# Optimization experiments

Measured on AMD Instinct MI355X. Metric: run time of the kernel, lower is better.

The kernel has to match this reference:

```python
import jax, jax.numpy as jnp
import numpy as np
import math

B, QLEN, KLEN = 8, 128, 1024
KDIM = QDIM = ADIM = ODIM = 512
HM, HC = 4, 4            # monotonic / chunkwise heads
CHUNK = 4                # chunkwise attention window
EPS = 1e-6
SHARPENING = 1.0
NEG_INF = float(np.finfo(np.float32).min)


def moving_sum(x, back, forward):
    """Windowed sum over last axis: out[k] = sum_{j=k-back}^{k+forward} x[j].
    Equivalent to the conv1d-with-ones-filter moving_sum in the torch code."""
    K = x.shape[-1]
    xp = jnp.pad(x, [(0, 0)] * (x.ndim - 1) + [(back, forward)])
    cs = jnp.cumsum(xp, axis=-1)
    L = back + forward + 1
    upper = jax.lax.slice_in_dim(cs, L - 1, L - 1 + K, axis=-1)
    lower = jnp.concatenate([jnp.zeros_like(cs[..., :1]),
                             jax.lax.slice_in_dim(cs, 0, K - 1, axis=-1)], axis=-1)
    return upper - lower


def safe_cumprod(x, eps):
    """exp(exclusive_cumsum(log(clip(x, eps, 1)))) along last axis."""
    logx = jnp.log(jnp.clip(x, eps, 1.0))
    excl = jnp.concatenate([jnp.zeros_like(logx[..., :1]),
                            jnp.cumsum(logx, axis=-1)[..., :-1]], axis=-1)
    return jnp.exp(excl)


def _heads(x, w, b, h):
    y = x @ w + b                                   # [B, L, ADIM]
    bs, L, _ = y.shape
    return y.reshape(bs, L, h, -1).transpose(0, 2, 1, 3)  # [B, h, L, d_k]


def setup_inputs() -> dict:
    key = jax.random.key(0)
    ks = jax.random.split(key, 16)
    s = 0.02
    f32 = jnp.float32
    return {
        "key_x": jax.random.normal(ks[0], (B, KLEN, KDIM), f32),
        "query_x": jax.random.normal(ks[1], (B, QLEN, QDIM), f32),
        "mask": jnp.ones((B, QLEN, KLEN), jnp.int32),
        "wk_m": jax.random.normal(ks[2], (KDIM, ADIM), f32) * s,
        "bk_m": jnp.zeros((ADIM,), f32),
        "wq_m": jax.random.normal(ks[3], (QDIM, ADIM), f32) * s,
        "bq_m": jnp.zeros((ADIM,), f32),
        "r": jnp.asarray(-4.0, f32),
        "wk_c": jax.random.normal(ks[4], (KDIM, ADIM), f32) * s,
        "bk_c": jnp.zeros((ADIM,), f32),
        "wq_c": jax.random.normal(ks[5], (QDIM, ADIM), f32) * s,
        "bq_c": jnp.zeros((ADIM,), f32),
        "wv": jax.random.normal(ks[6], (KDIM, ADIM), f32) * s,
        "bv": jnp.zeros((ADIM,), f32),
        "wo": jax.random.normal(ks[7], (ADIM, ODIM), f32) * s,
        "bo": jnp.zeros((ODIM,), f32),
    }


def reference(key_x, query_x, mask, wk_m, bk_m, wq_m, bq_m, r,
              wk_c, bk_c, wq_c, bq_c, wv, bv, wo, bo):
    scale = math.sqrt(ADIM)
    m = (mask[:, None] > 0)                                    # [B,1,Q,K]

    # ---- monotonic energy (scaled_dot + offset r) ----
    km = _heads(key_x, wk_m, bk_m, HM)                         # [B,HM,K,dk]
    qm = _heads(query_x, wq_m, bq_m, HM)                       # [B,HM,Q,dk]
    e_mono = jnp.einsum('bhqd,bhkd->bhqk', qm, km) / scale + r
    e_mono = jnp.where(m, e_mono, NEG_INF)

    # ---- monotonic alpha via safe_cumprod + per-step cumsum recurrence ----
    p_choose = jax.nn.sigmoid(e_mono)                          # [B,HM,Q,K]
    cp = safe_cumprod(1.0 - p_choose, EPS)                     # [B,HM,Q,K]
    aw0 = jnp.zeros((B, HM, KLEN), e_mono.dtype).at[..., 0].set(1.0)

    def step(aw_prev, pc):
        p_i, cp_i = pc                                         # [B,HM,K]
        aw = p_i * cp_i * jnp.cumsum(aw_prev / jnp.maximum(cp_i, EPS), axis=-1)
        return aw, aw

    _, alpha = jax.lax.scan(step, aw0,
                            (p_choose.transpose(2, 0, 1, 3),
                             cp.transpose(2, 0, 1, 3)))
    alpha = alpha.transpose(1, 2, 0, 3)                        # [B,HM,Q,K]

    # ---- chunkwise energy ----
    kc = _heads(key_x, wk_c, bk_c, HC)
    qc = _heads(query_x, wq_c, bq_c, HC)
    e_chunk = jnp.einsum('bhqd,bhkd->bhqk', qc, kc) / scale
    e_chunk = jnp.where(m, e_chunk, NEG_INF)

    # ---- efficient chunkwise attention (clipped-logit trick) ----
    e = e_chunk - jnp.max(e_chunk, axis=-1, keepdims=True)
    sexp = jnp.maximum(jnp.exp(e), 1e-5)[:, None]              # [B,1,HC,Q,K]
    denom = moving_sum(sexp, CHUNK - 1, 0)                     # [B,1,HC,Q,K]
    beta = sexp * moving_sum(alpha[:, :, None] * SHARPENING / denom,
                             0, CHUNK - 1)                     # [B,HM,HC,Q,K]
    beta = beta.reshape(B, HM * HC, QLEN, KLEN)

    # ---- context + output projection ----
    v = (key_x @ wv + bv).reshape(B, KLEN, HM * HC, ADIM // (HM * HC))
    cv = jnp.einsum('bhqk,bkhd->bqhd', beta, v).reshape(B, QLEN, ADIM)
    return cv @ wo + bo
```

## Files before the change

### kernel.cpp

```cpp
#include <hip/hip_runtime.h>
#include <hip/hip_bf16.h>


#define NEG_INF (-3.402823466e38f)
#define EPS_MOCHA 1e-6f
#define INV_SCALE 0.04419417382415922f

typedef _Float16 half8 __attribute__((ext_vector_type(8)));
typedef _Float16 half4v __attribute__((ext_vector_type(4)));
typedef float f32x4 __attribute__((ext_vector_type(4)));

#define WAITBAR(N) asm volatile("s_waitcnt vmcnt(" #N ") lgkmcnt(0)\n\ts_barrier" ::: "memory")
#define BARLG() asm volatile("s_waitcnt lgkmcnt(0)\n\ts_barrier" ::: "memory")

__device__ __forceinline__ float frcp(float x) { return __builtin_amdgcn_rcpf(x); }

__device__ __forceinline__ float wave_incl_scan(float x)
{
    int v;
    v = __builtin_amdgcn_update_dpp(0, __builtin_bit_cast(int, x), 0x111, 0xF, 0xF, false);
    x += __builtin_bit_cast(float, v);
    v = __builtin_amdgcn_update_dpp(0, __builtin_bit_cast(int, x), 0x112, 0xF, 0xF, false);
    x += __builtin_bit_cast(float, v);
    v = __builtin_amdgcn_update_dpp(0, __builtin_bit_cast(int, x), 0x114, 0xF, 0xF, false);
    x += __builtin_bit_cast(float, v);
    v = __builtin_amdgcn_update_dpp(0, __builtin_bit_cast(int, x), 0x118, 0xF, 0xF, false);
    x += __builtin_bit_cast(float, v);
    v = __builtin_amdgcn_update_dpp(0, __builtin_bit_cast(int, x), 0x142, 0xA, 0xF, false);
    x += __builtin_bit_cast(float, v);
    v = __builtin_amdgcn_update_dpp(0, __builtin_bit_cast(int, x), 0x143, 0xC, 0xF, false);
    x += __builtin_bit_cast(float, v);
    return x;
}

__device__ __forceinline__ half8 cvt8(float4 a, float4 b)
{
    half8 h = {(_Float16)a.x, (_Float16)a.y, (_Float16)a.z, (_Float16)a.w,
               (_Float16)b.x, (_Float16)b.y, (_Float16)b.z, (_Float16)b.w};
    return h;
}

__global__ __launch_bounds__(256) void prep_all(
    const float* __restrict__ wk_m, const float* __restrict__ wk_c,
    const float* __restrict__ wv, const float* __restrict__ wq_m,
    const float* __restrict__ wq_c, const float* __restrict__ wo,
    const float* __restrict__ key_x, const float* __restrict__ query_x,
    _Float16* __restrict__ Wt5, _Float16* __restrict__ Wt_wo,
    _Float16* __restrict__ X16)
{
    __shared__ float T[64][65];
    const int bid = blockIdx.x;
    const int t = threadIdx.x;
    if (bid < 384) {
        const int z = bid >> 6, w = bid & 63;
        const float* W = (z == 0) ? wk_m : (z == 1) ? wk_c : (z == 2) ? wv
                       : (z == 3) ? wq_m : (z == 4) ? wq_c : wo;
        _Float16* O = (z < 5) ? (Wt5 + (size_t)z * 262144) : Wt_wo;
        const int n0 = (w & 7) * 64, k0 = (w >> 3) * 64;
        const int rr = t >> 4, cc = (t & 15) * 4;
#pragma unroll
        for (int r = 0; r < 4; ++r) {
            int k = r * 16 + rr;
            float4 v = *(const float4*)(W + (size_t)(k0 + k) * 512 + n0 + cc);
            T[k][cc + 0] = v.x; T[k][cc + 1] = v.y;
            T[k][cc + 2] = v.z; T[k][cc + 3] = v.w;
        }
        __syncthreads();
        const int nn = t >> 2, kc = (t & 3) * 16;
        _Float16 tmp[16];
#pragma unroll
        for (int i = 0; i < 16; ++i) tmp[i] = (_Float16)T[kc + i][nn];
        _Float16* Op = O + (size_t)(n0 + nn) * 512 + k0 + kc;
        *(half8*)(Op)     = *(half8*)&tmp[0];
        *(half8*)(Op + 8) = *(half8*)&tmp[8];
    } else {
        const size_t KELEMS = (size_t)8192 * 512;
        size_t o = ((size_t)(bid - 384) * 256 + t) * 8;
        const float* s = (o < KELEMS) ? (key_x + o) : (query_x + (o - KELEMS));
        float4 a = *(const float4*)s;
        float4 b = *(const float4*)(s + 4);
        *(half8*)(X16 + o) = cvt8(a, b);
    }
}

__device__ __forceinline__ void stage16(const _Float16* src, _Float16* dst)
{
    __builtin_amdgcn_global_load_lds(
        (const __attribute__((address_space(1))) void*)src,
        (__attribute__((address_space(3))) void*)dst, 16, 0, 0);
}

template <int NSTEPS>
__device__ __forceinline__ void gemm8_f16(
    const _Float16* __restrict__ Abase, const _Float16* __restrict__ Bbase,
    _Float16* As, _Float16* Bs, f32x4 acc[4][2])
{
    const int tid = threadIdx.x;
    const int lane = tid & 63, wave = tid >> 6;
    const int wm = wave >> 2, wn = wave & 3;
    const int col = lane & 15, quad = lane >> 4;
    const int r0 = tid >> 2, seg = tid & 3;

    const _Float16* Ag = Abase + (size_t)r0 * 512 + seg * 8;
    const _Float16* Bg = Bbase + (size_t)r0 * 512 + seg * 8;

    stage16(Ag, As + tid * 8);
    stage16(Bg, Bs + tid * 8);
    if (NSTEPS > 1) {
        stage16(Ag + 32, As + 4096 + tid * 8);
        stage16(Bg + 32, Bs + 4096 + tid * 8);
        WAITBAR(2);
    } else {
        WAITBAR(0);
    }

#pragma unroll
    for (int ks = 0; ks < NSTEPS; ++ks) {
        const int cur = ks % 3;
        if (ks + 2 < NSTEPS) {
            const int s2 = (ks + 2) % 3;
            stage16(Ag + (ks + 2) * 32, As + s2 * 4096 + tid * 8);
            stage16(Bg + (ks + 2) * 32, Bs + s2 * 4096 + tid * 8);
        }
        const _Float16* Afr = As + cur * 4096 + (size_t)(wm * 64 + col) * 32 + quad * 8;
        const _Float16* Bfr = Bs + cur * 4096 + (size_t)(wn * 32 + col) * 32 + quad * 8;
        half8 a[4], b[2];
#pragma unroll
        for (int t = 0; t < 4; ++t) a[t] = *(const half8*)(Afr + (size_t)t * 16 * 32);
#pragma unroll
        for (int t = 0; t < 2; ++t) b[t] = *(const half8*)(Bfr + (size_t)t * 16 * 32);
#pragma unroll
        for (int mt = 0; mt < 4; ++mt)
#pragma unroll
            for (int nt = 0; nt < 2; ++nt)
                acc[mt][nt] = __builtin_amdgcn_mfma_f32_16x16x32_f16(
                    a[mt], b[nt], acc[mt][nt], 0, 0, 0);
        if (ks + 2 < NSTEPS)      WAITBAR(2);
        else if (ks + 1 < NSTEPS) WAITBAR(0);
    }
}

__device__ __forceinline__ void proj_epilogue8(
    f32x4 acc[4][2], const float* __restrict__ bias, void* __restrict__ Cv,
    int m0, int n0, int f16o)
{
    const int tid = threadIdx.x;
    const int lane = tid & 63, wave = tid >> 6;
    const int wm = wave >> 2, wn = wave & 3;
    const int col = lane & 15, quad = lane >> 4;
    float bnt[2];
#pragma unroll
    for (int nt = 0; nt < 2; ++nt)
        bnt[nt] = bias[n0 + wn * 32 + nt * 16 + col];
#pragma unroll
    for (int mt = 0; mt < 4; ++mt) {
        const int rowb = m0 + wm * 64 + mt * 16 + quad * 4;
#pragma unroll
        for (int nt = 0; nt < 2; ++nt) {
            const int cc = n0 + wn * 32 + nt * 16 + col;
#pragma unroll
            for (int r = 0; r < 4; ++r) {
                float v = acc[mt][nt][r] + bnt[nt];
                if (f16o)
                    ((_Float16*)Cv)[(size_t)(rowb + r) * 512 + cc] = (_Float16)v;
                else
                    ((float*)Cv)[(size_t)(rowb + r) * 512 + cc] = v;
            }
        }
    }
}

__global__ __launch_bounds__(512, 8) void mfma_proj5(
    const _Float16* __restrict__ X16, const _Float16* __restrict__ Wt5,
    const float* __restrict__ b0, void* __restrict__ C0,
    const float* __restrict__ b1, void* __restrict__ C1,
    const float* __restrict__ b2, void* __restrict__ C2,
    const float* __restrict__ b3, void* __restrict__ C3,
    const float* __restrict__ b4, void* __restrict__ C4)
{
    __shared__ _Float16 As[12288];
    __shared__ _Float16 Bs[12288];
    const int bid = (blockIdx.x & 7) * 104 + (blockIdx.x >> 3);
    int g, mblk, nblk;
    if (bid < 768) {
        g = bid >> 8; mblk = (bid & 255) >> 2; nblk = bid & 3;
    } else {
        const int t = bid - 768;
        g = 3 + (t >> 5); mblk = (t & 31) >> 2; nblk = t & 3;
    }
    const bool qry = g >= 3;
    const _Float16* A = X16 + (qry ? (size_t)8192 * 512 : 0);
    const _Float16* Wt = Wt5 + (size_t)g * 262144;
    const float* bias = (g == 0) ? b0 : (g == 1) ? b1 : (g == 2) ? b2
                      : (g == 3) ? b3 : b4;
    void* Cv = (g == 0) ? C0 : (g == 1) ? C1 : (g == 2) ? C2
             : (g == 3) ? C3 : C4;
    const int m0 = mblk * 128, n0 = nblk * 128;

    f32x4 acc[4][2];
#pragma unroll
    for (int mt = 0; mt < 4; ++mt)
#pragma unroll
        for (int nt = 0; nt < 2; ++nt) acc[mt][nt] = (f32x4)0.f;
    gemm8_f16<16>(A + (size_t)m0 * 512, Wt + (size_t)n0 * 512, As, Bs, acc);
    proj_epilogue8(acc, bias, Cv, m0, n0, 1);
}

__global__ __launch_bounds__(512, 4) void mfma_proj_out(
    const _Float16* __restrict__ A16, const _Float16* __restrict__ Wt,
    const float* __restrict__ bias, float* __restrict__ C)
{
    __shared__ _Float16 As[12288];
    __shared__ _Float16 Bs[12288];
    const int m0 = blockIdx.x * 128, n0 = blockIdx.y * 128;
    f32x4 acc[4][2];
#pragma unroll
    for (int mt = 0; mt < 4; ++mt)
#pragma unroll
        for (int nt = 0; nt < 2; ++nt) acc[mt][nt] = (f32x4)0.f;
    gemm8_f16<16>(A16 + (size_t)m0 * 512, Wt + (size_t)n0 * 512, As, Bs, acc);
    proj_epilogue8(acc, bias, C, m0, n0, 0);
}

__global__ __launch_bounds__(512, 4) void energy_mfma(
    const _Float16* __restrict__ Qm, const _Float16* __restrict__ Km,
    const _Float16* __restrict__ Qc, const _Float16* __restrict__ Kc,
    const int* __restrict__ mask, float* __restrict__ e_mono,
    _Float16* __restrict__ e_chunk16, const float* __restrict__ r_ptr)
{
    __shared__ _Float16 As[12288];
    __shared__ _Float16 Bs[12288];
    const int tid = threadIdx.x;
    const int lane = tid & 63, wave = tid >> 6;
    const int wm = wave >> 2, wn = wave & 3;
    const int col = lane & 15, quad = lane >> 4;
    const int kt0 = blockIdx.x * 128;
    const int h = blockIdx.y;
    const int b = blockIdx.z;
    const float rv = r_ptr[0];
    const int r0 = tid >> 2, seg = tid & 3;

    const _Float16* Am0 = Qm + (size_t)(b * 128) * 512 + h * 128 + (size_t)r0 * 512 + seg * 8;
    const _Float16* Ac0 = Qc + (size_t)(b * 128) * 512 + h * 128 + (size_t)r0 * 512 + seg * 8;
    const _Float16* Bm0 = Km + (size_t)(b * 1024 + kt0) * 512 + h * 128 + (size_t)r0 * 512 + seg * 8;
    const _Float16* Bc0 = Kc + (size_t)(b * 1024 + kt0) * 512 + h * 128 + (size_t)r0 * 512 + seg * 8;
#define EGA(s) (((s) < 4 ? Am0 : Ac0) + ((s) & 3) * 32)
#define EGB(s) (((s) < 4 ? Bm0 : Bc0) + ((s) & 3) * 32)

    f32x4 accM[4][2], accC[4][2];
#pragma unroll
    for (int mt = 0; mt < 4; ++mt)
#pragma unroll
        for (int nt = 0; nt < 2; ++nt) { accM[mt][nt] = (f32x4)0.f; accC[mt][nt] = (f32x4)0.f; }

#pragma unroll
    for (int s = 0; s < 2; ++s) {
        stage16(EGA(s), As + s * 4096 + tid * 8);
        stage16(EGB(s), Bs + s * 4096 + tid * 8);
    }
    WAITBAR(2);

#pragma unroll
    for (int ks = 0; ks < 8; ++ks) {
        const int cur = ks % 3;
        if (ks + 2 < 8) {
            const int s2 = (ks + 2) % 3;
            stage16(EGA(ks + 2), As + s2 * 4096 + tid * 8);
            stage16(EGB(ks + 2), Bs + s2 * 4096 + tid * 8);
        }
        const _Float16* Afr = As + cur * 4096 + (size_t)(wm * 64 + col) * 32 + quad * 8;
        const _Float16* Bfr = Bs + cur * 4096 + (size_t)(wn * 32 + col) * 32 + quad * 8;
        half8 a[4], bf[2];
#pragma unroll
        for (int t = 0; t < 4; ++t) a[t]  = *(const half8*)(Afr + (size_t)t * 16 * 32);
#pragma unroll
        for (int t = 0; t < 2; ++t) bf[t] = *(const half8*)(Bfr + (size_t)t * 16 * 32);
        if (ks < 4) {
#pragma unroll
            for (int mt = 0; mt < 4; ++mt)
#pragma unroll
                for (int nt = 0; nt < 2; ++nt)
                    accM[mt][nt] = __builtin_amdgcn_mfma_f32_16x16x32_f16(a[mt], bf[nt], accM[mt][nt], 0, 0, 0);
        } else {
#pragma unroll
            for (int mt = 0; mt < 4; ++mt)
#pragma unroll
                for (int nt = 0; nt < 2; ++nt)
                    accC[mt][nt] = __builtin_amdgcn_mfma_f32_16x16x32_f16(a[mt], bf[nt], accC[mt][nt], 0, 0, 0);
        }
        if (ks + 2 < 8)      WAITBAR(2);
        else if (ks + 1 < 8) WAITBAR(0);
    }
#undef EGA
#undef EGB

#pragma unroll
    for (int mt = 0; mt < 4; ++mt) {
        const int qb = wm * 64 + mt * 16 + quad * 4;
#pragma unroll
        for (int nt = 0; nt < 2; ++nt) {
            const int kc = kt0 + wn * 32 + nt * 16 + col;
#pragma unroll
            for (int r = 0; r < 4; ++r) {
                const int q = qb + r;
                const int mv = mask[((size_t)b * 128 + q) * 1024 + kc];
                const size_t oi = (((size_t)b * 4 + h) * 128 + q) * 1024 + kc;
                float vm = accM[mt][nt][r] * INV_SCALE + rv;
                e_mono[oi] = mv ? vm : NEG_INF;
                float vc = accC[mt][nt][r] * INV_SCALE;
                e_chunk16[oi] = (_Float16)(mv ? vc : NEG_INF);
            }
        }
    }
}

__device__ __forceinline__ void transcend_row(
    const float* __restrict__ Erow, int lane, float o_pcp[16], float o_inv[16])
{
    const float* E = Erow + lane * 16;
    float e[16];
    *(float4*)&e[0]  = *(const float4*)(E);
    *(float4*)&e[4]  = *(const float4*)(E + 4);
    *(float4*)&e[8]  = *(const float4*)(E + 8);
    *(float4*)&e[12] = *(const float4*)(E + 12);

    float p[16], l[16];
#pragma unroll
    for (int i = 0; i < 16; ++i) {
        p[i] = frcp(1.f + __expf(-e[i]));
        l[i] = __logf(fmaxf(1.f - p[i], EPS_MOCHA));
    }
    float incl[16];
    incl[0] = l[0];
#pragma unroll
    for (int i = 1; i < 16; ++i) incl[i] = incl[i - 1] + l[i];
    float total = incl[15];
    float x = wave_incl_scan(total);
    float base = x - total;
#pragma unroll
    for (int i = 0; i < 16; ++i) {
        float cl = base + (i ? incl[i - 1] : 0.f);
        float cp = __expf(cl);
        o_pcp[i] = p[i] * cp;
        o_inv[i] = frcp(fmaxf(cp, EPS_MOCHA));
    }
}

#define SW2(k) ((k) + ((k) >> 4))

__global__ __launch_bounds__(512) void alpha_pre(
    const float* __restrict__ e_mono, float* __restrict__ G,
    float* __restrict__ pcp)
{
    __shared__ float pshare[8][1088];
    const int tid = threadIdx.x;
    const int lane = tid & 63;
    const int wid = tid >> 6;
    const int row = blockIdx.x * 8 + wid;
    const int q = row & 127;

    float pq[16], iq[16];
    transcend_row(e_mono + (size_t)row * 1024, lane, pq, iq);

    float* P = pcp + (size_t)row * 1024 + lane * 16;
    *(float4*)(P)      = *(float4*)&pq[0];
    *(float4*)(P + 4)  = *(float4*)&pq[4];
    *(float4*)(P + 8)  = *(float4*)&pq[8];
    *(float4*)(P + 12) = *(float4*)&pq[12];

#pragma unroll
    for (int i = 0; i < 16; ++i)
        pshare[wid][SW2(lane * 16 + i)] = pq[i];
    __syncthreads();

    float g[16];
    if (q == 0) {
#pragma unroll
        for (int i = 0; i < 16; ++i) g[i] = 0.f;
        if (lane == 0) g[0] = iq[0];
    } else if (wid > 0) {
#pragma unroll
        for (int i = 0; i < 16; ++i)
            g[i] = pshare[wid - 1][SW2(lane * 16 + i)] * iq[i];
    } else {
        float pm[16], im[16];
        transcend_row(e_mono + (size_t)(row - 1) * 1024, lane, pm, im);
#pragma unroll
        for (int i = 0; i < 16; ++i) g[i] = pm[i] * iq[i];
    }
    float* Gp = G + (size_t)row * 1024 + lane * 16;
    *(float4*)(Gp)      = *(float4*)&g[0];
    *(float4*)(Gp + 4)  = *(float4*)&g[4];
    *(float4*)(Gp + 8)  = *(float4*)&g[8];
    *(float4*)(Gp + 12) = *(float4*)&g[12];
}

__global__ __launch_bounds__(256) void alpha_scan(
    const float* __restrict__ G, float* __restrict__ S)
{
    __shared__ float carry[2][4];
    const int tid = threadIdx.x;
    const int lane = tid & 63, wid = tid >> 6;
    const int bh = blockIdx.x;
    const float* Gp = G + (size_t)bh * 131072 + tid * 4;
    float* Sp = S + (size_t)bh * 131072 + tid * 4;

    float4 g0 = *(const float4*)(Gp);
    float4 g1 = *(const float4*)(Gp + 1024);
    float4 g2 = *(const float4*)(Gp + 2048);
    float4 g3 = *(const float4*)(Gp + 3072);

    float Sv0 = 1.f, Sv1 = 1.f, Sv2 = 1.f, Sv3 = 1.f;

#define SCAN_STEP(GV, QQ)                                                    \
    {                                                                        \
        float i0 = GV.x * Sv0;                                               \
        float i1 = fmaf(GV.y, Sv1, i0);                                      \
        float i2 = fmaf(GV.z, Sv2, i1);                                      \
        float i3 = fmaf(GV.w, Sv3, i2);                                      \
        float x = wave_incl_scan(i3);                                        \
        float base = x - i3;                                                 \
        if (lane == 63) carry[(QQ) & 1][wid] = x;                            \
        BARLG();                                                             \
        float pre = 0.f;                                                     \
        if (wid > 0) pre += carry[(QQ) & 1][0];                              \
        if (wid > 1) pre += carry[(QQ) & 1][1];                              \
        if (wid > 2) pre += carry[(QQ) & 1][2];                              \
        float ba = pre + base;                                               \
        Sv0 = ba + i0; Sv1 = ba + i1; Sv2 = ba + i2; Sv3 = ba + i3;          \
        float4 sv = {Sv0, Sv1, Sv2, Sv3};                                    \
        *(float4*)(Sp + (size_t)(QQ) * 1024) = sv;                           \
    }

    for (int q = 0; q < 128; q += 4) {
        SCAN_STEP(g0, q);
        if (q + 4 < 128) g0 = *(const float4*)(Gp + (size_t)(q + 4) * 1024);
        SCAN_STEP(g1, q + 1);
        if (q + 5 < 128) g1 = *(const float4*)(Gp + (size_t)(q + 5) * 1024);
        SCAN_STEP(g2, q + 2);
        if (q + 6 < 128) g2 = *(const float4*)(Gp + (size_t)(q + 6) * 1024);
        SCAN_STEP(g3, q + 3);
        if (q + 7 < 128) g3 = *(const float4*)(Gp + (size_t)(q + 7) * 1024);
    }
#undef SCAN_STEP
}

__global__ __launch_bounds__(256) void beta_kernel(
    const _Float16* __restrict__ e_chunk16, const float* __restrict__ pcp,
    const float* __restrict__ S, _Float16* __restrict__ beta)
{
    __shared__ float red[4];
    __shared__ float edge_sx[4][4];
    __shared__ float edge_t[4][4][4];
    const int q = blockIdx.x, b = blockIdx.y;
    const int tid = threadIdx.x;
    const int lane = tid & 63, wid = tid >> 6;
    const int k4 = tid * 4;

    float av[4][4];
#pragma unroll
    for (int hm = 0; hm < 4; ++hm) {
        const size_t off = (((size_t)b * 4 + hm) * 128 + q) * 1024 + k4;
        float4 pv = *(const float4*)(pcp + off);
        float4 sv = *(const float4*)(S + off);
        av[hm][0] = pv.x * sv.x;
        av[hm][1] = pv.y * sv.y;
        av[hm][2] = pv.z * sv.z;
        av[hm][3] = pv.w * sv.w;
    }

    for (int hc = 0; hc < 4; ++hc) {
        half4v ev = *(const half4v*)(e_chunk16 + (((size_t)b * 4 + hc) * 128 + q) * 1024 + k4);
        float e[4] = {(float)ev[0], (float)ev[1], (float)ev[2], (float)ev[3]};

        float mx = fmaxf(fmaxf(e[0], e[1]), fmaxf(e[2], e[3]));
#pragma unroll
        for (int off = 32; off >= 1; off >>= 1)
            mx = fmaxf(mx, __shfl_xor(mx, off, 64));
        if (lane == 0) red[wid] = mx;
        __syncthreads();
        mx = fmaxf(fmaxf(red[0], red[1]), fmaxf(red[2], red[3]));

        float sx[4];
#pragma unroll
        for (int i = 0; i < 4; ++i)
            sx[i] = fmaxf(__expf(e[i] - mx), 1e-5f);
        if (lane == 63) {
            edge_sx[wid][0] = sx[0]; edge_sx[wid][1] = sx[1];
            edge_sx[wid][2] = sx[2]; edge_sx[wid][3] = sx[3];
        }
        __syncthreads();

        float p1 = __shfl_up(sx[3], 1, 64);
        float p2 = __shfl_up(sx[2], 1, 64);
        float p3 = __shfl_up(sx[1], 1, 64);
        if (lane == 0) {
            if (wid > 0) {
                p1 = edge_sx[wid - 1][3];
                p2 = edge_sx[wid - 1][2];
                p3 = edge_sx[wid - 1][1];
            } else {
                p1 = 0.f; p2 = 0.f; p3 = 0.f;
            }
        }
        float den[4];
        den[0] = sx[0] + p1 + p2 + p3;
        den[1] = sx[1] + sx[0] + p1 + p2;
        den[2] = sx[2] + sx[1] + sx[0] + p1;
        den[3] = sx[3] + sx[2] + sx[1] + sx[0];
        float rd[4];
#pragma unroll
        for (int i = 0; i < 4; ++i) rd[i] = frcp(den[i]);

        float t[4][4];
#pragma unroll
        for (int hm = 0; hm < 4; ++hm)
#pragma unroll
            for (int i = 0; i < 4; ++i)
                t[hm][i] = av[hm][i] * rd[i];
        if (lane == 0) {
#pragma unroll
            for (int hm = 0; hm < 4; ++hm) {
                edge_t[wid][hm][0] = t[hm][0]; edge_t[wid][hm][1] = t[hm][1];
                edge_t[wid][hm][2] = t[hm][2]; edge_t[wid][hm][3] = t[hm][3];
            }
        }
        __syncthreads();

#pragma unroll
        for (int hm = 0; hm < 4; ++hm) {
            float n1 = __shfl_down(t[hm][0], 1, 64);
            float n2 = __shfl_down(t[hm][1], 1, 64);
            float n3 = __shfl_down(t[hm][2], 1, 64);
            if (lane == 63) {
                if (wid < 3) {
                    n1 = edge_t[wid + 1][hm][0];
                    n2 = edge_t[wid + 1][hm][1];
                    n3 = edge_t[wid + 1][hm][2];
                } else {
                    n1 = 0.f; n2 = 0.f; n3 = 0.f;
                }
            }
            float o0 = sx[0] * (t[hm][0] + t[hm][1] + t[hm][2] + t[hm][3]);
            float o1 = sx[1] * (t[hm][1] + t[hm][2] + t[hm][3] + n1);
            float o2 = sx[2] * (t[hm][2] + t[hm][3] + n1 + n2);
            float o3 = sx[3] * (t[hm][3] + n1 + n2 + n3);
            _Float16* Brow = beta + (((size_t)b * 16 + hm * 4 + hc) * 128 + q) * 1024;
            half4v hv = {(_Float16)o0, (_Float16)o1, (_Float16)o2, (_Float16)o3};
            *(half4v*)(Brow + k4) = hv;
        }
    }
}

__global__ __launch_bounds__(256) void context_kernel(
    const _Float16* __restrict__ beta, const _Float16* __restrict__ V16,
    _Float16* __restrict__ cv16)
{
    __shared__ float bS[128][64];
    __shared__ float vS[128][32];
    const int qh = blockIdx.x, h = blockIdx.y, b = blockIdx.z;
    const int tid = threadIdx.x;
    const int ty = tid >> 3, tx = tid & 7;
    const int q0 = qh * 64;

    const _Float16* Bbase = beta + (((size_t)b * 16 + h) * 128 + q0) * 1024;
    const _Float16* Vbase = V16 + (size_t)b * 1024 * 512 + h * 32;

    float acc[2][4];
#pragma unroll
    for (int i = 0; i < 2; ++i)
#pragma unroll
        for (int j = 0; j < 4; ++j) acc[i][j] = 0.f;

    for (int k0 = 0; k0 < 1024; k0 += 128) {
        {
            int r = tid >> 2, c = tid & 3;
#pragma unroll
            for (int s = 0; s < 4; ++s) {
                half8 v = *(const half8*)(Bbase + (size_t)r * 1024 + k0 + s * 32 + c * 8);
#pragma unroll
                for (int j = 0; j < 8; ++j) bS[s * 32 + c * 8 + j][r] = (float)v[j];
            }
        }
        {
            int kk = tid >> 3, c = tid & 7;
#pragma unroll
            for (int s = 0; s < 4; ++s) {
                half4v v = *(const half4v*)(Vbase + (size_t)(k0 + s * 32 + kk) * 512 + c * 4);
                float4 f = {(float)v[0], (float)v[1], (float)v[2], (float)v[3]};
                *(float4*)&vS[s * 32 + kk][c * 4] = f;
            }
        }
        __syncthreads();
#pragma unroll 8
        for (int kk = 0; kk < 128; ++kk) {
            float a0 = bS[kk][ty * 2], a1 = bS[kk][ty * 2 + 1];
            float bb[4];
            *(float4*)bb = *(const float4*)&vS[kk][tx * 4];
#pragma unroll
            for (int j = 0; j < 4; ++j) {
                acc[0][j] = fmaf(a0, bb[j], acc[0][j]);
                acc[1][j] = fmaf(a1, bb[j], acc[1][j]);
            }
        }
        __syncthreads();
    }
#pragma unroll
    for (int i = 0; i < 2; ++i) {
        _Float16* Cp = cv16 + ((size_t)b * 128 + q0 + ty * 2 + i) * 512 + h * 32 + tx * 4;
        half4v hv = {(_Float16)acc[i][0], (_Float16)acc[i][1],
                     (_Float16)acc[i][2], (_Float16)acc[i][3]};
        *(half4v*)Cp = hv;
    }
}

extern "C" void kernel_launch(void* const* d_in, const int* in_sizes, int n_in,
                              void* d_out, int out_size, void* d_ws, size_t ws_size,
                              hipStream_t stream)
{
    const float* key_x   = (const float*)d_in[0];
    const float* query_x = (const float*)d_in[1];
    const int*   mask    = (const int*)d_in[2];
    const float* wk_m = (const float*)d_in[3];
    const float* bk_m = (const float*)d_in[4];
    const float* wq_m = (const float*)d_in[5];
    const float* bq_m = (const float*)d_in[6];
    const float* r    = (const float*)d_in[7];
    const float* wk_c = (const float*)d_in[8];
    const float* bk_c = (const float*)d_in[9];
    const float* wq_c = (const float*)d_in[10];
    const float* bq_c = (const float*)d_in[11];
    const float* wv   = (const float*)d_in[12];
    const float* bv   = (const float*)d_in[13];
    const float* wo   = (const float*)d_in[14];
    const float* bo   = (const float*)d_in[15];
    float* out = (float*)d_out;

    float* ws = (float*)d_ws;
    _Float16* hws = (_Float16*)d_ws;
    const size_t MEGF = 1024 * 1024;
    _Float16* Km16  = hws;
    _Float16* Kc16  = hws + 4 * MEGF;
    _Float16* Qm16  = hws + 8 * MEGF;
    _Float16* Qc16  = hws + 8 * MEGF + 524288;
    _Float16* X16   = hws + 16 * MEGF;
    float* e_mono  = ws + 11 * MEGF;
    _Float16* e_chunk16 = hws + 34 * MEGF;
    _Float16* V16  = hws + 38 * MEGF;
    float* G       = ws;
    float* pcp     = ws + 4 * MEGF;
    float* S       = ws + 23 * MEGF;
    _Float16* beta16 = hws + 16 * MEGF;
    _Float16* Wt5   = hws + 54 * MEGF;
    _Float16* Wt_wo = hws + 54 * MEGF + 5 * 262144;
    _Float16* cv16  = hws + 55 * MEGF + MEGF / 2;

    prep_all<<<dim3(2688), 256, 0, stream>>>(
        wk_m, wk_c, wv, wq_m, wq_c, wo, key_x, query_x, Wt5, Wt_wo, X16);
    mfma_proj5<<<dim3(832), 512, 0, stream>>>(
        X16, Wt5, bk_m, Km16, bk_c, Kc16, bv, V16, bq_m, Qm16, bq_c, Qc16);
    energy_mfma<<<dim3(8, 4, 8), 512, 0, stream>>>(
        Qm16, Km16, Qc16, Kc16, mask, e_mono, e_chunk16, r);
    alpha_pre<<<dim3(512), 512, 0, stream>>>(e_mono, G, pcp);
    alpha_scan<<<dim3(32), 256, 0, stream>>>(G, S);
    beta_kernel<<<dim3(128, 8), 256, 0, stream>>>(e_chunk16, pcp, S, beta16);
    context_kernel<<<dim3(2, 16, 8), 256, 0, stream>>>(beta16, V16, cv16);
    mfma_proj_out<<<dim3(8, 4), 512, 0, stream>>>(cv16, Wt_wo, bo, out);
}
```

Measured before the change: 243.2 us.

## Split energy kernel per head type, compress mask to bytes, widen context blocks

Three changes land together. The energy kernel now launches separate blocks for the monotonic and chunkwise energies, doubling the grid and reusing the shared gemm8_f16 path instead of one block computing both. The int32 mask is packed into bytes inside the prep kernel, so the energy epilogue reads a quarter of the mask bytes. The context kernel moves to 512 threads with one output row per thread and padded shared arrays to reduce bank conflicts. The cost is an extra mask-conversion pass in prep and duplicated Q/K tile staging addresses across the split blocks.

New measurement: 243.8 us. Within noise of the previous version (+0.3%).

```diff
diff --git a/kernel.cpp b/kernel.cpp
--- a/kernel.cpp
+++ b/kernel.cpp
@@ -45,8 +45,9 @@
     const float* __restrict__ wv, const float* __restrict__ wq_m,
     const float* __restrict__ wq_c, const float* __restrict__ wo,
     const float* __restrict__ key_x, const float* __restrict__ query_x,
+    const int* __restrict__ mask,
     _Float16* __restrict__ Wt5, _Float16* __restrict__ Wt_wo,
-    _Float16* __restrict__ X16)
+    _Float16* __restrict__ X16, signed char* __restrict__ mask8)
 {
     __shared__ float T[64][65];
     const int bid = blockIdx.x;
@@ -73,13 +74,28 @@
         _Float16* Op = O + (size_t)(n0 + nn) * 512 + k0 + kc;
         *(half8*)(Op)     = *(half8*)&tmp[0];
         *(half8*)(Op + 8) = *(half8*)&tmp[8];
-    } else {
+    } else if (bid < 2688) {
         const size_t KELEMS = (size_t)8192 * 512;
         size_t o = ((size_t)(bid - 384) * 256 + t) * 8;
         const float* s = (o < KELEMS) ? (key_x + o) : (query_x + (o - KELEMS));
         float4 a = *(const float4*)s;
         float4 b = *(const float4*)(s + 4);
         *(half8*)(X16 + o) = cvt8(a, b);
+    } else {
+        size_t o = ((size_t)(bid - 2688) * 256 + t) * 8;
+        const int* mp = mask + o;
+        int4 a = *(const int4*)mp;
+        int4 b = *(const int4*)(mp + 4);
+        unsigned long long pk = 0;
+        pk |= (unsigned long long)(a.x != 0) << 0;
+        pk |= (unsigned long long)(a.y != 0) << 8;
+        pk |= (unsigned long long)(a.z != 0) << 16;
+        pk |= (unsigned long long)(a.w != 0) << 24;
+        pk |= (unsigned long long)(b.x != 0) << 32;
+        pk |= (unsigned long long)(b.y != 0) << 40;
+        pk |= (unsigned long long)(b.z != 0) << 48;
+        pk |= (unsigned long long)(b.w != 0) << 56;
+        *(unsigned long long*)(mask8 + o) = pk;
     }
 }
 
@@ -225,7 +241,7 @@
 __global__ __launch_bounds__(512, 4) void energy_mfma(
     const _Float16* __restrict__ Qm, const _Float16* __restrict__ Km,
     const _Float16* __restrict__ Qc, const _Float16* __restrict__ Kc,
-    const int* __restrict__ mask, float* __restrict__ e_mono,
+    const signed char* __restrict__ mask8, float* __restrict__ e_mono,
     _Float16* __restrict__ e_chunk16, const float* __restrict__ r_ptr)
 {
     __shared__ _Float16 As[12288];
@@ -236,63 +252,20 @@
     const int col = lane & 15, quad = lane >> 4;
     const int kt0 = blockIdx.x * 128;
     const int h = blockIdx.y;
-    const int b = blockIdx.z;
-    const float rv = r_ptr[0];
-    const int r0 = tid >> 2, seg = tid & 3;
-
-    const _Float16* Am0 = Qm + (size_t)(b * 128) * 512 + h * 128 + (size_t)r0 * 512 + seg * 8;
-    const _Float16* Ac0 = Qc + (size_t)(b * 128) * 512 + h * 128 + (size_t)r0 * 512 + seg * 8;
-    const _Float16* Bm0 = Km + (size_t)(b * 1024 + kt0) * 512 + h * 128 + (size_t)r0 * 512 + seg * 8;
-    const _Float16* Bc0 = Kc + (size_t)(b * 1024 + kt0) * 512 + h * 128 + (size_t)r0 * 512 + seg * 8;
-#define EGA(s) (((s) < 4 ? Am0 : Ac0) + ((s) & 3) * 32)
-#define EGB(s) (((s) < 4 ? Bm0 : Bc0) + ((s) & 3) * 32)
-
-    f32x4 accM[4][2], accC[4][2];
+    const int z = blockIdx.z;
+    const int b = z & 7;
+    const bool mono = z < 8;
+    const _Float16* Qp = mono ? Qm : Qc;
+    const _Float16* Kp = mono ? Km : Kc;
+    const float rv = mono ? r_ptr[0] : 0.f;
+
+    f32x4 acc[4][2];
 #pragma unroll
     for (int mt = 0; mt < 4; ++mt)
 #pragma unroll
-        for (int nt = 0; nt < 2; ++nt) { accM[mt][nt] = (f32x4)0.f; accC[mt][nt] = (f32x4)0.f; }
-
-#pragma unroll
-    for (int s = 0; s < 2; ++s) {
-        stage16(EGA(s), As + s * 4096 + tid * 8);
-        stage16(EGB(s), Bs + s * 4096 + tid * 8);
-    }
-    WAITBAR(2);
-
-#pragma unroll
-    for (int ks = 0; ks < 8; ++ks) {
-        const int cur = ks % 3;
-        if (ks + 2 < 8) {
-            const int s2 = (ks + 2) % 3;
-            stage16(EGA(ks + 2), As + s2 * 4096 + tid * 8);
-            stage16(EGB(ks + 2), Bs + s2 * 4096 + tid * 8);
-        }
-        const _Float16* Afr = As + cur * 4096 + (size_t)(wm * 64 + col) * 32 + quad * 8;
-        const _Float16* Bfr = Bs + cur * 4096 + (size_t)(wn * 32 + col) * 32 + quad * 8;
-        half8 a[4], bf[2];
-#pragma unroll
-        for (int t = 0; t < 4; ++t) a[t]  = *(const half8*)(Afr + (size_t)t * 16 * 32);
-#pragma unroll
-        for (int t = 0; t < 2; ++t) bf[t] = *(const half8*)(Bfr + (size_t)t * 16 * 32);
-        if (ks < 4) {
-#pragma unroll
-            for (int mt = 0; mt < 4; ++mt)
-#pragma unroll
-                for (int nt = 0; nt < 2; ++nt)
-                    accM[mt][nt] = __builtin_amdgcn_mfma_f32_16x16x32_f16(a[mt], bf[nt], accM[mt][nt], 0, 0, 0);
-        } else {
-#pragma unroll
-            for (int mt = 0; mt < 4; ++mt)
-#pragma unroll
-                for (int nt = 0; nt < 2; ++nt)
-                    accC[mt][nt] = __builtin_amdgcn_mfma_f32_16x16x32_f16(a[mt], bf[nt], accC[mt][nt], 0, 0, 0);
-        }
-        if (ks + 2 < 8)      WAITBAR(2);
-        else if (ks + 1 < 8) WAITBAR(0);
-    }
-#undef EGA
-#undef EGB
+        for (int nt = 0; nt < 2; ++nt) acc[mt][nt] = (f32x4)0.f;
+    gemm8_f16<4>(Qp + (size_t)(b * 128) * 512 + h * 128,
+                 Kp + (size_t)(b * 1024 + kt0) * 512 + h * 128, As, Bs, acc);
 
 #pragma unroll
     for (int mt = 0; mt < 4; ++mt) {
@@ -303,12 +276,11 @@
 #pragma unroll
             for (int r = 0; r < 4; ++r) {
                 const int q = qb + r;
-                const int mv = mask[((size_t)b * 128 + q) * 1024 + kc];
+                const int mv = mask8[((size_t)b * 128 + q) * 1024 + kc];
                 const size_t oi = (((size_t)b * 4 + h) * 128 + q) * 1024 + kc;
-                float vm = accM[mt][nt][r] * INV_SCALE + rv;
-                e_mono[oi] = mv ? vm : NEG_INF;
-                float vc = accC[mt][nt][r] * INV_SCALE;
-                e_chunk16[oi] = (_Float16)(mv ? vc : NEG_INF);
+                float v = acc[mt][nt][r] * INV_SCALE + rv;
+                if (mono) e_mono[oi] = mv ? v : NEG_INF;
+                else      e_chunk16[oi] = (_Float16)(mv ? v : NEG_INF);
             }
         }
     }
@@ -552,66 +524,59 @@
     }
 }
 
-__global__ __launch_bounds__(256) void context_kernel(
+__global__ __launch_bounds__(512) void context_kernel(
     const _Float16* __restrict__ beta, const _Float16* __restrict__ V16,
     _Float16* __restrict__ cv16)
 {
-    __shared__ float bS[128][64];
-    __shared__ float vS[128][32];
+    __shared__ float bS[128][65];
+    __shared__ float vS[128][36];
     const int qh = blockIdx.x, h = blockIdx.y, b = blockIdx.z;
     const int tid = threadIdx.x;
-    const int ty = tid >> 3, tx = tid & 7;
+    const int ty = tid >> 3;
+    const int tx = tid & 7;
     const int q0 = qh * 64;
 
     const _Float16* Bbase = beta + (((size_t)b * 16 + h) * 128 + q0) * 1024;
     const _Float16* Vbase = V16 + (size_t)b * 1024 * 512 + h * 32;
 
-    float acc[2][4];
-#pragma unroll
-    for (int i = 0; i < 2; ++i)
-#pragma unroll
-        for (int j = 0; j < 4; ++j) acc[i][j] = 0.f;
+    float acc[4] = {0.f, 0.f, 0.f, 0.f};
 
     for (int k0 = 0; k0 < 1024; k0 += 128) {
         {
-            int r = tid >> 2, c = tid & 3;
-#pragma unroll
-            for (int s = 0; s < 4; ++s) {
-                half8 v = *(const half8*)(Bbase + (size_t)r * 1024 + k0 + s * 32 + c * 8);
-#pragma unroll
-                for (int j = 0; j < 8; ++j) bS[s * 32 + c * 8 + j][r] = (float)v[j];
+            const int r = tid >> 3, c = tid & 7;
+            half8 v0 = *(const half8*)(Bbase + (size_t)r * 1024 + k0 + c * 16);
+            half8 v1 = *(const half8*)(Bbase + (size_t)r * 1024 + k0 + c * 16 + 8);
+#pragma unroll
+            for (int j = 0; j < 8; ++j) {
+                bS[c * 16 + j][r]     = (float)v0[j];
+                bS[c * 16 + 8 + j][r] = (float)v1[j];
             }
         }
         {
-            int kk = tid >> 3, c = tid & 7;
-#pragma unroll
-            for (int s = 0; s < 4; ++s) {
-                half4v v = *(const half4v*)(Vbase + (size_t)(k0 + s * 32 + kk) * 512 + c * 4);
-                float4 f = {(float)v[0], (float)v[1], (float)v[2], (float)v[3]};
-                *(float4*)&vS[s * 32 + kk][c * 4] = f;
+            const int kk = tid >> 2, cc = tid & 3;
+            half4v w0 = *(const half4v*)(Vbase + (size_t)(k0 + kk) * 512 + cc * 8);
+            half4v w1 = *(const half4v*)(Vbase + (size_t)(k0 + kk) * 512 + cc * 8 + 4);
+#pragma unroll
+            for (int j = 0; j < 4; ++j) {
+                vS[kk][cc * 8 + j]     = (float)w0[j];
+                vS[kk][cc * 8 + 4 + j] = (float)w1[j];
             }
         }
         __syncthreads();
 #pragma unroll 8
         for (int kk = 0; kk < 128; ++kk) {
-            float a0 = bS[kk][ty * 2], a1 = bS[kk][ty * 2 + 1];
+            float a = bS[kk][ty];
             float bb[4];
             *(float4*)bb = *(const float4*)&vS[kk][tx * 4];
 #pragma unroll
-            for (int j = 0; j < 4; ++j) {
-                acc[0][j] = fmaf(a0, bb[j], acc[0][j]);
-                acc[1][j] = fmaf(a1, bb[j], acc[1][j]);
-            }
+            for (int j = 0; j < 4; ++j) acc[j] = fmaf(a, bb[j], acc[j]);
         }
         __syncthreads();
     }
-#pragma unroll
-    for (int i = 0; i < 2; ++i) {
-        _Float16* Cp = cv16 + ((size_t)b * 128 + q0 + ty * 2 + i) * 512 + h * 32 + tx * 4;
-        half4v hv = {(_Float16)acc[i][0], (_Float16)acc[i][1],
-                     (_Float16)acc[i][2], (_Float16)acc[i][3]};
-        *(half4v*)Cp = hv;
-    }
+    _Float16* Cp = cv16 + ((size_t)b * 128 + q0 + ty) * 512 + h * 32 + tx * 4;
+    half4v hv = {(_Float16)acc[0], (_Float16)acc[1],
+                 (_Float16)acc[2], (_Float16)acc[3]};
+    *(half4v*)Cp = hv;
 }
 
 extern "C" void kernel_launch(void* const* d_in, const int* in_sizes, int n_in,
@@ -644,6 +609,7 @@
     _Float16* Qm16  = hws + 8 * MEGF;
     _Float16* Qc16  = hws + 8 * MEGF + 524288;
     _Float16* X16   = hws + 16 * MEGF;
+    signed char* mask8 = (signed char*)(hws + 20 * MEGF + MEGF / 2);
     float* e_mono  = ws + 11 * MEGF;
     _Float16* e_chunk16 = hws + 34 * MEGF;
     _Float16* V16  = hws + 38 * MEGF;
@@ -655,15 +621,16 @@
     _Float16* Wt_wo = hws + 54 * MEGF + 5 * 262144;
     _Float16* cv16  = hws + 55 * MEGF + MEGF / 2;
 
-    prep_all<<<dim3(2688), 256, 0, stream>>>(
-        wk_m, wk_c, wv, wq_m, wq_c, wo, key_x, query_x, Wt5, Wt_wo, X16);
+    prep_all<<<dim3(3200), 256, 0, stream>>>(
+        wk_m, wk_c, wv, wq_m, wq_c, wo, key_x, query_x, mask,
+        Wt5, Wt_wo, X16, mask8);
     mfma_proj5<<<dim3(832), 512, 0, stream>>>(
         X16, Wt5, bk_m, Km16, bk_c, Kc16, bv, V16, bq_m, Qm16, bq_c, Qc16);
-    energy_mfma<<<dim3(8, 4, 8), 512, 0, stream>>>(
-        Qm16, Km16, Qc16, Kc16, mask, e_mono, e_chunk16, r);
+    energy_mfma<<<dim3(8, 4, 16), 512, 0, stream>>>(
+        Qm16, Km16, Qc16, Kc16, mask8, e_mono, e_chunk16, r);
     alpha_pre<<<dim3(512), 512, 0, stream>>>(e_mono, G, pcp);
     alpha_scan<<<dim3(32), 256, 0, stream>>>(G, S);
     beta_kernel<<<dim3(128, 8), 256, 0, stream>>>(e_chunk16, pcp, S, beta16);
-    context_kernel<<<dim3(2, 16, 8), 256, 0, stream>>>(beta16, V16, cv16);
+    context_kernel<<<dim3(2, 16, 8), 512, 0, stream>>>(beta16, V16, cv16);
     mfma_proj_out<<<dim3(8, 4), 512, 0, stream>>>(cv16, Wt_wo, bo, out);
 }
```
